# Optimization experiments

Measured on AMD Instinct MI355X. Metric: run time of the kernel, lower is better.

## Reference

```python
import jax, jax.numpy as jnp
import numpy as np

D_MODEL = 1024
D_STATE = 128
HEADDIM = 64
EXPAND = 2
CHUNK = 64
D_CONV = 4
D_INNER = EXPAND * D_MODEL          # 2048
NHEADS = D_INNER // HEADDIM         # 32
D_IN_PROJ = 2 * D_INNER + 2 * D_STATE + NHEADS  # 4384
CONV_CH = D_INNER + 2 * D_STATE     # 2304
EPS = 1e-5


def segsum(x):
    # x: (..., T) -> (..., T, T); out[i, j] = sum_{k=j+1..i} x[k] for i>=j else -inf
    T = x.shape[-1]
    m1 = jnp.tril(jnp.ones((T, T), bool), -1)
    xr = jnp.where(m1, x[..., :, None], 0.0)   # zero above/at diagonal before cumsum
    s = jnp.cumsum(xr, axis=-2)
    m0 = jnp.tril(jnp.ones((T, T), bool), 0)
    return jnp.where(m0, s, -jnp.inf)


def ssd(x, A, B, C, chunk):
    # x: (b, L, h, p); A: (b, L, h); B, C: (b, L, n)  (the h=1 dim of the torch code is squeezed)
    b, L, h, p = x.shape
    c = L // chunk
    x = x.reshape(b, c, chunk, h, p)
    A = A.reshape(b, c, chunk, h).transpose(0, 3, 1, 2)  # (b, h, c, l)
    B = B.reshape(b, c, chunk, -1)                       # (b, c, l, n)
    C = C.reshape(b, c, chunk, -1)
    A_cum = jnp.cumsum(A, axis=-1)                       # (b, h, c, l)
    Lm = jnp.exp(segsum(A))                              # (b, h, c, l, l)
    # intra-chunk (diagonal block) output
    Y_diag = jnp.einsum('bcln,bcsn,bhcls,bcshp->bclhp', C, B, Lm, x)
    # per-chunk states
    decay_states = jnp.exp(A_cum[:, :, :, -1:] - A_cum)  # (b, h, c, l)
    states = jnp.einsum('bcln,bhcl,bclhp->bchpn', B, decay_states, x)
    init = jnp.zeros_like(states[:, :1])
    states = jnp.concatenate([init, states], axis=1)     # (b, c+1, h, p, n)
    # inter-chunk recurrence
    Ac_last = jnp.pad(A_cum[:, :, :, -1], ((0, 0), (0, 0), (1, 0)))  # (b, h, c+1)
    decay_chunk = jnp.exp(segsum(Ac_last))               # (b, h, c+1, c+1)
    new_states = jnp.einsum('bhzc,bchpn->bzhpn', decay_chunk, states)
    states = new_states[:, :-1]                          # (b, c, h, p, n)
    sdo = jnp.exp(A_cum)
    Y_off = jnp.einsum('bcln,bchpn,bhcl->bclhp', C, states, sdo)
    return (Y_diag + Y_off).reshape(b, L, h, p)


def setup_inputs() -> dict:
    key = jax.random.key(0)
    ks = jax.random.split(key, 8)
    return {
        'u': jax.random.normal(ks[0], (2, 4096, D_MODEL), jnp.float32),
        'W_in': jax.random.normal(ks[1], (D_MODEL, D_IN_PROJ), jnp.float32) * 0.02,
        'conv_w': jax.random.normal(ks[2], (CONV_CH, D_CONV), jnp.float32) * 0.3,
        'conv_b': jax.random.normal(ks[3], (CONV_CH,), jnp.float32) * 0.1,
        'dt_bias': jax.random.normal(ks[4], (NHEADS,), jnp.float32),
        'A_log': jax.random.normal(ks[5], (NHEADS,), jnp.float32) * 0.5,
        'D': jax.random.normal(ks[6], (NHEADS,), jnp.float32),
        'norm_w': jnp.ones((D_INNER,), jnp.float32),
        'W_out': jax.random.normal(ks[7], (D_INNER, D_MODEL), jnp.float32) * 0.02,
    }


def reference(u, W_in, conv_w, conv_b, dt_bias, A_log, D, norm_w, W_out):
    b, L, _ = u.shape
    zxbcdt = u @ W_in                                    # (b, L, 4384)
    z = zxbcdt[..., :D_INNER]
    xBC = zxbcdt[..., D_INNER:D_INNER + CONV_CH]
    dt = jax.nn.softplus(zxbcdt[..., -NHEADS:] + dt_bias)  # (b, L, h)
    # depthwise causal conv (Conv1d pad=d_conv-1, truncated to L == left-pad only)
    xc = jnp.pad(xBC.transpose(0, 2, 1), ((0, 0), (0, 0), (D_CONV - 1, 0)))
    xc = jax.lax.conv_general_dilated(
        xc, conv_w[:, None, :], (1,), 'VALID',
        feature_group_count=CONV_CH,
        dimension_numbers=('NCH', 'OIH', 'NCH')) + conv_b[None, :, None]
    xBC = jax.nn.silu(xc.transpose(0, 2, 1))             # (b, L, 2304)
    x = xBC[..., :D_INNER].reshape(b, L, NHEADS, HEADDIM)
    B = xBC[..., D_INNER:D_INNER + D_STATE]
    C = xBC[..., D_INNER + D_STATE:]
    A = -jnp.exp(A_log)                                  # (h,)
    y = ssd(x * dt[..., None], A * dt, B, C, CHUNK)
    y = y + x * D[:, None]
    y = y.reshape(b, L, D_INNER)
    # RMSNorm with gate z
    y = y * jax.nn.silu(z)
    y = y * jax.lax.rsqrt(jnp.mean(y * y, axis=-1, keepdims=True) + EPS) * norm_w
    return y @ W_out
```

## Files before the change

kernel.cpp:

```cpp
#include <hip/hip_runtime.h>
#include <hip/hip_bf16.h>
#include <math.h>

#define D_MODEL   1024
#define D_STATE   128
#define HEADDIM   64
#define CHUNK     64
#define D_INNER   2048
#define NHEADS    32
#define D_IN_PROJ 4384
#define CONV_CH   2304
#define RCOLS     2336
#define WINT_ROWS 4480
#define BATCH     2
#define SEQ       4096
#define NCHUNK    64
#define ROWS      (BATCH*SEQ)
#define EPS_RMS   1e-5f

typedef __hip_bfloat16 bf16;
typedef __bf16 bf16x8_t __attribute__((ext_vector_type(8)));
typedef float  f32x4_t  __attribute__((ext_vector_type(4)));

__device__ __forceinline__ float siluf_(float x){ return x/(1.f+expf(-x)); }
__device__ __forceinline__ float ldf(const float* p){ return *p; }
__device__ __forceinline__ float ldf(const bf16* p){ return __bfloat162float(*p); }
__device__ __forceinline__ void  stf(float* p, float v){ *p = v; }
__device__ __forceinline__ void  stf(bf16* p, float v){ *p = __float2bfloat16(v); }

__device__ __forceinline__ __bf16 tobf(float v){
    __hip_bfloat16 t = __float2bfloat16(v);
    return *reinterpret_cast<__bf16*>(&t);
}
__device__ __forceinline__ unsigned short bfbits(float v){
    __hip_bfloat16 t = __float2bfloat16(v);
    return *reinterpret_cast<unsigned short*>(&t);
}
__device__ __forceinline__ float bfbits2f(unsigned short u){
    union { unsigned u; float f; } cv; cv.u = ((unsigned)u) << 16; return cv.f;
}

__device__ __forceinline__ void async16(const void* g, void* l) {
    __builtin_amdgcn_global_load_lds(
        (const __attribute__((address_space(1))) unsigned int*)g,
        (__attribute__((address_space(3))) unsigned int*)l, 16, 0, 0);
}

struct GemmCore {
    f32x4_t acc[4][4];
    __device__ __forceinline__ void run(const bf16* __restrict__ A, int lda,
                                        const bf16* __restrict__ Bt, int ldb,
                                        int row0, int col0, int k0, int k1,
                                        __bf16* As, __bf16* Bs,
                                        int wave, int lane) {
        const int quad = lane >> 4, l16 = lane & 15;
        const int wr = (wave >> 1) * 64, wc = (wave & 1) * 64;
#pragma unroll
        for (int i = 0; i < 4; ++i)
#pragma unroll
            for (int j = 0; j < 4; ++j) acc[i][j] = (f32x4_t){0.f, 0.f, 0.f, 0.f};
        const int ca0 = wave * 2, ca1 = wave * 2 + 1;
        const int srow = lane >> 2, scol = (lane & 3) * 8;
        const bf16* Ag0 = A  + (size_t)(row0 + ca0 * 16 + srow) * lda + scol;
        const bf16* Ag1 = A  + (size_t)(row0 + ca1 * 16 + srow) * lda + scol;
        const bf16* Bg0 = Bt + (size_t)(col0 + ca0 * 16 + srow) * ldb + scol;
        const bf16* Bg1 = Bt + (size_t)(col0 + ca1 * 16 + srow) * ldb + scol;
        __bf16* Al0 = As + ca0 * 512;
        __bf16* Al1 = As + ca1 * 512;
        __bf16* Bl0 = Bs + ca0 * 512;
        __bf16* Bl1 = Bs + ca1 * 512;
        for (int kk = k0; kk < k1; kk += 32) {
            async16(Ag0 + kk, Al0);
            async16(Ag1 + kk, Al1);
            async16(Bg0 + kk, Bl0);
            async16(Bg1 + kk, Bl1);
            __syncthreads();
            bf16x8_t af[4], bfr[4];
#pragma unroll
            for (int mi = 0; mi < 4; ++mi)
                af[mi] = *(const bf16x8_t*)(As + (wr + mi * 16 + l16) * 32 + quad * 8);
#pragma unroll
            for (int ni = 0; ni < 4; ++ni)
                bfr[ni] = *(const bf16x8_t*)(Bs + (wc + ni * 16 + l16) * 32 + quad * 8);
#pragma unroll
            for (int mi = 0; mi < 4; ++mi)
#pragma unroll
                for (int ni = 0; ni < 4; ++ni)
                    acc[mi][ni] = __builtin_amdgcn_mfma_f32_16x16x32_bf16(
                        af[mi], bfr[ni], acc[mi][ni], 0, 0, 0);
            __syncthreads();
        }
    }
};

__global__ __launch_bounds__(256) void gemm_zr_fused(const bf16* __restrict__ A,
                                                     const bf16* __restrict__ Bt,
                                                     bf16* __restrict__ Z,
                                                     bf16* __restrict__ R) {
    __shared__ __align__(16) __bf16 As[128 * 32];
    __shared__ __align__(16) __bf16 Bs[128 * 32];
    const int tid = threadIdx.x, wave = tid >> 6, lane = tid & 63;
    const int quad = lane >> 4, l16 = lane & 15;
    const int row0 = blockIdx.x * 128;
    const int ct   = blockIdx.y;
    GemmCore g;
    g.run(A, D_MODEL, Bt, D_MODEL, row0, ct * 128, 0, D_MODEL, As, Bs, wave, lane);

    bf16* Cp; int ldc_, cl0, ncols;
    if (ct < 16) { Cp = Z; ldc_ = D_INNER; cl0 = ct * 128;          ncols = D_INNER; }
    else         { Cp = R; ldc_ = RCOLS;   cl0 = ct * 128 - D_INNER; ncols = RCOLS; }
    const int wr = (wave >> 1) * 64, wc = (wave & 1) * 64;
#pragma unroll
    for (int ni = 0; ni < 4; ++ni) {
        int gc = cl0 + wc + ni * 16 + l16;
        if (gc >= ncols) continue;
#pragma unroll
        for (int mi = 0; mi < 4; ++mi)
#pragma unroll
            for (int r = 0; r < 4; ++r) {
                int gr = row0 + wr + mi * 16 + quad * 4 + r;
                stf(&Cp[(size_t)gr * ldc_ + gc], g.acc[mi][ni][r]);
            }
    }
}

__global__ __launch_bounds__(256) void gemm_out_splitk(const bf16* __restrict__ A,
                                                       const bf16* __restrict__ Bt,
                                                       float* __restrict__ part) {
    __shared__ __align__(16) __bf16 As[128 * 32];
    __shared__ __align__(16) __bf16 Bs[128 * 32];
    const int tid = threadIdx.x, wave = tid >> 6, lane = tid & 63;
    const int quad = lane >> 4, l16 = lane & 15;
    const int row0 = blockIdx.x * 128;
    const int col0 = blockIdx.y * 128;
    const int kz   = blockIdx.z;
    GemmCore g;
    g.run(A, D_INNER, Bt, D_INNER, row0, col0, kz * 1024, kz * 1024 + 1024,
          As, Bs, wave, lane);
    float* P = part + (size_t)kz * ROWS * D_MODEL;
    const int wr = (wave >> 1) * 64, wc = (wave & 1) * 64;
#pragma unroll
    for (int ni = 0; ni < 4; ++ni) {
        int gc = col0 + wc + ni * 16 + l16;
#pragma unroll
        for (int mi = 0; mi < 4; ++mi)
#pragma unroll
            for (int r = 0; r < 4; ++r) {
                int gr = row0 + wr + mi * 16 + quad * 4 + r;
                P[(size_t)gr * D_MODEL + gc] = g.acc[mi][ni][r];
            }
    }
}

__global__ void reduce_out_kernel(const float* __restrict__ part,
                                  float* __restrict__ out) {
    int i = blockIdx.x * 256 + threadIdx.x;
    float4 a = ((const float4*)part)[i];
    float4 b = ((const float4*)(part + (size_t)ROWS * D_MODEL))[i];
    ((float4*)out)[i] = make_float4(a.x + b.x, a.y + b.y, a.z + b.z, a.w + b.w);
}

__global__ void cvt_bf16_kernel(const float* __restrict__ src,
                                bf16* __restrict__ dst, int n4) {
    int i = blockIdx.x * 256 + threadIdx.x;
    if (i >= n4) return;
    float4 v = ((const float4*)src)[i];
    dst[i * 4 + 0] = __float2bfloat16(v.x);
    dst[i * 4 + 1] = __float2bfloat16(v.y);
    dst[i * 4 + 2] = __float2bfloat16(v.z);
    dst[i * 4 + 3] = __float2bfloat16(v.w);
}

__global__ __launch_bounds__(256) void transpose_cvt_kernel(const float* __restrict__ W,
                                                            bf16* __restrict__ Wt,
                                                            int R, int C, int Cpad) {
    __shared__ float tile[32][33];
    int c0 = blockIdx.x * 32, r0 = blockIdx.y * 32;
    int tx = threadIdx.x & 31, ty = threadIdx.x >> 5;
    for (int i = ty; i < 32; i += 8) {
        int r = r0 + i, c = c0 + tx;
        tile[i][tx] = (c < C) ? W[(size_t)r * C + c] : 0.f;
    }
    __syncthreads();
    for (int i = ty; i < 32; i += 8) {
        int c = c0 + i, r = r0 + tx;
        stf(&Wt[(size_t)c * R + r], tile[tx][i]);
    }
}

__global__ void prep_convw_kernel(const float* __restrict__ conv_w,
                                  bf16* __restrict__ Wc) {
    int i = blockIdx.x * 256 + threadIdx.x;
    if (i >= CONV_CH * 4) return;
    int ch = i >> 2, k = i & 3;
    Wc[k * CONV_CH + ch] = __float2bfloat16(conv_w[ch * 4 + k]);
}

__global__ __launch_bounds__(256) void conv_silu_kernel(const bf16* __restrict__ R,
                                                        const bf16* __restrict__ Wc,
                                                        const float* __restrict__ conv_b,
                                                        bf16* __restrict__ xBC) {
    int idx = blockIdx.x * 256 + threadIdx.x;
    int rq = idx / 288;
    int g = idx - rq * 288;
    int ch0 = g * 8;
    int row0 = rq * 4;
    int l0 = row0 & (SEQ - 1);

    uint4 rv[7];
#pragma unroll
    for (int j = 0; j < 7; ++j) {
        int ls = l0 - 3 + j;
        rv[j] = (ls >= 0) ? *(const uint4*)&R[(size_t)(row0 - 3 + j) * RCOLS + ch0]
                          : make_uint4(0u, 0u, 0u, 0u);
    }
    uint4 wv[4];
#pragma unroll
    for (int k = 0; k < 4; ++k)
        wv[k] = *(const uint4*)&Wc[k * CONV_CH + ch0];
    float4 b0 = ((const float4*)conv_b)[ch0 / 4];
    float4 b1 = ((const float4*)conv_b)[ch0 / 4 + 1];
    const float bias[8] = {b0.x, b0.y, b0.z, b0.w, b1.x, b1.y, b1.z, b1.w};
    float wf[4][8];
#pragma unroll
    for (int k = 0; k < 4; ++k) {
        const unsigned* wp = (const unsigned*)&wv[k];
#pragma unroll
        for (int j2 = 0; j2 < 4; ++j2) {
            wf[k][2 * j2]     = bfbits2f((unsigned short)(wp[j2] & 0xffff));
            wf[k][2 * j2 + 1] = bfbits2f((unsigned short)(wp[j2] >> 16));
        }
    }
#pragma unroll
    for (int j = 0; j < 4; ++j) {
        float acc[8];
#pragma unroll
        for (int cc = 0; cc < 8; ++cc) acc[cc] = bias[cc];
#pragma unroll
        for (int k = 0; k < 4; ++k) {
            const unsigned* vp = (const unsigned*)&rv[j + k];
#pragma unroll
            for (int j2 = 0; j2 < 4; ++j2) {
                unsigned v = vp[j2];
                acc[2 * j2]     += wf[k][2 * j2]     * bfbits2f((unsigned short)(v & 0xffff));
                acc[2 * j2 + 1] += wf[k][2 * j2 + 1] * bfbits2f((unsigned short)(v >> 16));
            }
        }
        unsigned o[4];
#pragma unroll
        for (int j2 = 0; j2 < 4; ++j2)
            o[j2] = (unsigned)bfbits(siluf_(acc[2 * j2])) |
                    ((unsigned)bfbits(siluf_(acc[2 * j2 + 1])) << 16);
        *(uint4*)&xBC[(size_t)(row0 + j) * CONV_CH + ch0] = make_uint4(o[0], o[1], o[2], o[3]);
    }
}

__global__ void dt_kernel(const bf16* __restrict__ R,
                          const float* __restrict__ dt_bias,
                          float* __restrict__ dtb) {
    int i = blockIdx.x * 256 + threadIdx.x;
    int row = i >> 2, h0 = (i & 3) * 8;
    uint4 v = *(const uint4*)&R[(size_t)row * RCOLS + CONV_CH + h0];
    float4 bia0 = ((const float4*)dt_bias)[h0 / 4];
    float4 bia1 = ((const float4*)dt_bias)[h0 / 4 + 1];
    const unsigned vv[4] = {v.x, v.y, v.z, v.w};
    const float bb[8] = {bia0.x, bia0.y, bia0.z, bia0.w, bia1.x, bia1.y, bia1.z, bia1.w};
    float o[8];
#pragma unroll
    for (int j = 0; j < 4; ++j) {
        float a = bfbits2f((unsigned short)(vv[j] & 0xffff)) + bb[2*j];
        float c = bfbits2f((unsigned short)(vv[j] >> 16)) + bb[2*j+1];
        o[2*j]   = (a > 20.f) ? a : log1pf(expf(a));
        o[2*j+1] = (c > 20.f) ? c : log1pf(expf(c));
    }
    float* dp = &dtb[(size_t)row * NHEADS + h0];
    *(float4*)dp       = make_float4(o[0], o[1], o[2], o[3]);
    *(float4*)(dp + 4) = make_float4(o[4], o[5], o[6], o[7]);
}

__global__ void acum_kernel(const float* __restrict__ dtb,
                            const float* __restrict__ A_log,
                            float* __restrict__ Acum) {
    int bch = blockIdx.x;
    int h = bch & 31;
    int bc = bch >> 5;
    int c = bc & 63, b = bc >> 6;
    int row0 = b * SEQ + c * CHUNK;
    __shared__ float sh[64];
    int l = threadIdx.x;
    float Ah = -expf(A_log[h]);
    sh[l] = Ah * dtb[(size_t)(row0 + l) * NHEADS + h];
    __syncthreads();
    float s = 0.f;
    for (int j = 0; j <= l; ++j) s += sh[j];
    Acum[(size_t)bch * 64 + l] = s;
}

__global__ __launch_bounds__(64) void gchunk_mfma_kernel(const bf16* __restrict__ xBC,
                                                         float* __restrict__ Gbuf) {
    int bc = blockIdx.x;
    int c = bc & 63, b = bc >> 6;
    int row0 = b * SEQ + c * CHUNK;
    int lane = threadIdx.x;
    int quad = lane >> 4, l16 = lane & 15;

    f32x4_t acc[4][4];
#pragma unroll
    for (int i = 0; i < 4; ++i)
#pragma unroll
        for (int j = 0; j < 4; ++j) acc[i][j] = (f32x4_t){0.f, 0.f, 0.f, 0.f};

#pragma unroll
    for (int ks = 0; ks < 4; ++ks) {
        bf16x8_t a[4], bb[4];
#pragma unroll
        for (int mi = 0; mi < 4; ++mi)
            a[mi] = *(const bf16x8_t*)&xBC[(size_t)(row0 + mi * 16 + l16) * CONV_CH +
                                           D_INNER + D_STATE + ks * 32 + quad * 8];
#pragma unroll
        for (int ni = 0; ni < 4; ++ni)
            bb[ni] = *(const bf16x8_t*)&xBC[(size_t)(row0 + ni * 16 + l16) * CONV_CH +
                                            D_INNER + ks * 32 + quad * 8];
#pragma unroll
        for (int mi = 0; mi < 4; ++mi)
#pragma unroll
            for (int ni = 0; ni < 4; ++ni)
                acc[mi][ni] = __builtin_amdgcn_mfma_f32_16x16x32_bf16(
                    a[mi], bb[ni], acc[mi][ni], 0, 0, 0);
    }
#pragma unroll
    for (int ni = 0; ni < 4; ++ni) {
        int s = ni * 16 + l16;
#pragma unroll
        for (int mi = 0; mi < 4; ++mi)
#pragma unroll
            for (int r = 0; r < 4; ++r) {
                int l = mi * 16 + quad * 4 + r;
                Gbuf[(size_t)bc * 4096 + l * 64 + s] = acc[mi][ni][r];
            }
    }
}

__global__ __launch_bounds__(256) void states_mfma_kernel(const bf16* __restrict__ xBC,
                                                          const float* __restrict__ dtb,
                                                          const float* __restrict__ Acum,
                                                          bf16* __restrict__ states) {
    __shared__ __align__(16) __bf16 BsT[128 * 72];
    __shared__ __align__(16) __bf16 xdT[4][64 * 72];
    __shared__ float dtdec[4][64];
    int bcq = blockIdx.x;
    int hq = bcq & 7, bc = bcq >> 3;
    int c = bc & 63, b = bc >> 6;
    int tid = threadIdx.x, wave = tid >> 6, lane = tid & 63;
    int h = hq * 4 + wave;
    int bch = bc * 32 + h;
    int row0 = b * SEQ + c * CHUNK;
    int quad = lane >> 4, l16 = lane & 15;

    {
        float alast = Acum[(size_t)bch * 64 + 63];
        float a = Acum[(size_t)bch * 64 + lane];
        dtdec[wave][lane] = dtb[(size_t)(row0 + lane) * NHEADS + h] * expf(alast - a);
    }
    __syncthreads();
    for (int it = 0; it < 16; ++it) {
        int i2 = tid + 256 * it;
        int l = i2 >> 6;
        int n0 = (i2 & 63) * 2;
        unsigned v = *(const unsigned*)&xBC[(size_t)(row0 + l) * CONV_CH + D_INNER + n0];
        *(unsigned short*)&BsT[(n0    ) * 72 + l] = (unsigned short)(v & 0xffff);
        *(unsigned short*)&BsT[(n0 + 1) * 72 + l] = (unsigned short)(v >> 16);
    }
    for (int it = 0; it < 32; ++it) {
        int l = 2 * it + (lane >> 5);
        int p0 = (lane & 31) * 2;
        unsigned v = *(const unsigned*)&xBC[(size_t)(row0 + l) * CONV_CH + h * 64 + p0];
        float f = dtdec[wave][l];
        xdT[wave][(p0    ) * 72 + l] = tobf(bfbits2f((unsigned short)(v & 0xffff)) * f);
        xdT[wave][(p0 + 1) * 72 + l] = tobf(bfbits2f((unsigned short)(v >> 16)) * f);
    }
    __syncthreads();

    f32x4_t acc[4][8];
#pragma unroll
    for (int i = 0; i < 4; ++i)
#pragma unroll
        for (int j = 0; j < 8; ++j) acc[i][j] = (f32x4_t){0.f, 0.f, 0.f, 0.f};
#pragma unroll
    for (int ks = 0; ks < 2; ++ks) {
        bf16x8_t a[4], bb[8];
#pragma unroll
        for (int mi = 0; mi < 4; ++mi)
            a[mi] = *(const bf16x8_t*)(&xdT[wave][(mi * 16 + l16) * 72 + ks * 32 + quad * 8]);
#pragma unroll
        for (int ni = 0; ni < 8; ++ni)
            bb[ni] = *(const bf16x8_t*)(&BsT[(ni * 16 + l16) * 72 + ks * 32 + quad * 8]);
#pragma unroll
        for (int mi = 0; mi < 4; ++mi)
#pragma unroll
            for (int ni = 0; ni < 8; ++ni)
                acc[mi][ni] = __builtin_amdgcn_mfma_f32_16x16x32_bf16(
                    a[mi], bb[ni], acc[mi][ni], 0, 0, 0);
    }
#pragma unroll
    for (int ni = 0; ni < 8; ++ni) {
        int n = ni * 16 + l16;
#pragma unroll
        for (int mi = 0; mi < 4; ++mi)
#pragma unroll
            for (int r = 0; r < 4; ++r) {
                int p = mi * 16 + quad * 4 + r;
                stf(&states[(size_t)bch * 8192 + p * 128 + n], acc[mi][ni][r]);
            }
    }
}

__global__ void scan_kernel(const float* __restrict__ Acum,
                            bf16* __restrict__ states) {
    int i = blockIdx.x * 256 + threadIdx.x;
    int pn0 = (i & 2047) * 4;
    int bh = i >> 11;
    int h = bh & 31, b = bh >> 5;
    float carry[4] = {0.f, 0.f, 0.f, 0.f};
    for (int c = 0; c < NCHUNK; ++c) {
        int bch = (b * NCHUNK + c) * NHEADS + h;
        bf16* sp = &states[(size_t)bch * 8192 + pn0];
        uint2 v = *(const uint2*)sp;
        float s0 = bfbits2f((unsigned short)(v.x & 0xffff));
        float s1 = bfbits2f((unsigned short)(v.x >> 16));
        float s2 = bfbits2f((unsigned short)(v.y & 0xffff));
        float s3 = bfbits2f((unsigned short)(v.y >> 16));
        uint2 o;
        o.x = (unsigned)bfbits(carry[0]) | ((unsigned)bfbits(carry[1]) << 16);
        o.y = (unsigned)bfbits(carry[2]) | ((unsigned)bfbits(carry[3]) << 16);
        *(uint2*)sp = o;
        float dec = expf(Acum[(size_t)bch * 64 + 63]);
        carry[0] = carry[0] * dec + s0;
        carry[1] = carry[1] * dec + s1;
        carry[2] = carry[2] * dec + s2;
        carry[3] = carry[3] * dec + s3;
    }
}

__global__ __launch_bounds__(64) void y_mfma_kernel(const bf16* __restrict__ xBC,
                                                    const float* __restrict__ dtb,
                                                    const float* __restrict__ Acum,
                                                    const float* __restrict__ Gbuf,
                                                    const bf16* __restrict__ states,
                                                    const float* __restrict__ Dv,
                                                    bf16* __restrict__ y) {
    __shared__ __align__(16) __bf16 Mm[64 * 72];
    __shared__ __align__(16) __bf16 xsT[64 * 72];
    __shared__ float acs[64], dtss[64], sdos[64];
    int bch = blockIdx.x;
    int h = bch & 31, bc = bch >> 5;
    int c = bc & 63, b = bc >> 6;
    int row0 = b * SEQ + c * CHUNK;
    int lane = threadIdx.x;
    int quad = lane >> 4, l16 = lane & 15;

    {
        float a = Acum[(size_t)bch * 64 + lane];
        acs[lane] = a;
        sdos[lane] = expf(a);
        dtss[lane] = dtb[(size_t)(row0 + lane) * NHEADS + h];
    }
    __syncthreads();
    for (int l = 0; l < 64; ++l) {
        int s = lane;
        float d = acs[l] - acs[s];
        float g = (s <= l) ? Gbuf[(size_t)bc * 4096 + l * 64 + s] * dtss[s] : 0.f;
        float coef = g * expf((s <= l) ? d : 0.f);
        Mm[l * 72 + s] = tobf(coef);
    }
    for (int it = 0; it < 32; ++it) {
        int l = 2 * it + (lane >> 5);
        int p0 = (lane & 31) * 2;
        unsigned v = *(const unsigned*)&xBC[(size_t)(row0 + l) * CONV_CH + h * 64 + p0];
        *(unsigned short*)&xsT[(p0    ) * 72 + l] = (unsigned short)(v & 0xffff);
        *(unsigned short*)&xsT[(p0 + 1) * 72 + l] = (unsigned short)(v >> 16);
    }
    __syncthreads();

    f32x4_t acc[4][4];
#pragma unroll
    for (int i = 0; i < 4; ++i)
#pragma unroll
        for (int j = 0; j < 4; ++j) acc[i][j] = (f32x4_t){0.f, 0.f, 0.f, 0.f};

#pragma unroll
    for (int ks = 0; ks < 2; ++ks) {
        bf16x8_t a[4], bb[4];
#pragma unroll
        for (int mi = 0; mi < 4; ++mi)
            a[mi] = *(const bf16x8_t*)(&Mm[(mi * 16 + l16) * 72 + ks * 32 + quad * 8]);
#pragma unroll
        for (int ni = 0; ni < 4; ++ni)
            bb[ni] = *(const bf16x8_t*)(&xsT[(ni * 16 + l16) * 72 + ks * 32 + quad * 8]);
#pragma unroll
        for (int mi = 0; mi < 4; ++mi)
#pragma unroll
            for (int ni = 0; ni < 4; ++ni)
                acc[mi][ni] = __builtin_amdgcn_mfma_f32_16x16x32_bf16(
                    a[mi], bb[ni], acc[mi][ni], 0, 0, 0);
    }
    float sdo_mi[4];
#pragma unroll
    for (int mi = 0; mi < 4; ++mi) sdo_mi[mi] = sdos[mi * 16 + l16];
#pragma unroll
    for (int ks = 0; ks < 4; ++ks) {
        bf16x8_t a[4], bb[4];
#pragma unroll
        for (int mi = 0; mi < 4; ++mi) {
            const unsigned* cp = (const unsigned*)&xBC[(size_t)(row0 + mi * 16 + l16) * CONV_CH
                                                       + D_INNER + D_STATE + ks * 32 + quad * 8];
            float sc = sdo_mi[mi];
#pragma unroll
            for (int jj = 0; jj < 4; ++jj) {
                unsigned v = cp[jj];
                a[mi][2 * jj    ] = tobf(bfbits2f((unsigned short)(v & 0xffff)) * sc);
                a[mi][2 * jj + 1] = tobf(bfbits2f((unsigned short)(v >> 16)) * sc);
            }
        }
#pragma unroll
        for (int ni = 0; ni < 4; ++ni)
            bb[ni] = *(const bf16x8_t*)&states[(size_t)bch * 8192 + (ni * 16 + l16) * 128
                                               + ks * 32 + quad * 8];
#pragma unroll
        for (int mi = 0; mi < 4; ++mi)
#pragma unroll
            for (int ni = 0; ni < 4; ++ni)
                acc[mi][ni] = __builtin_amdgcn_mfma_f32_16x16x32_bf16(
                    a[mi], bb[ni], acc[mi][ni], 0, 0, 0);
    }
    float Dh = Dv[h];
#pragma unroll
    for (int ni = 0; ni < 4; ++ni) {
        int p = ni * 16 + l16;
#pragma unroll
        for (int mi = 0; mi < 4; ++mi)
#pragma unroll
            for (int r = 0; r < 4; ++r) {
                int l = mi * 16 + quad * 4 + r;
                float xv = bfbits2f(*(const unsigned short*)&xsT[p * 72 + l]);
                stf(&y[(size_t)(row0 + l) * D_INNER + h * 64 + p],
                    acc[mi][ni][r] + Dh * xv);
            }
    }
}

__global__ __launch_bounds__(256) void gate_norm_kernel(const bf16* __restrict__ Z,
                                                        const float* __restrict__ nw,
                                                        bf16* __restrict__ y) {
    int row = blockIdx.x;
    int tid = threadIdx.x;
    int col0 = tid * 8;
    uint4 zv = *(const uint4*)&Z[(size_t)row * D_INNER + col0];
    uint4 yv = *(const uint4*)&y[(size_t)row * D_INNER + col0];
    const unsigned zz[4] = {zv.x, zv.y, zv.z, zv.w};
    const unsigned yy[4] = {yv.x, yv.y, yv.z, yv.w};
    float vals[8];
    float local = 0.f;
#pragma unroll
    for (int j = 0; j < 4; ++j) {
        float z0 = bfbits2f((unsigned short)(zz[j] & 0xffff));
        float z1 = bfbits2f((unsigned short)(zz[j] >> 16));
        float y0 = bfbits2f((unsigned short)(yy[j] & 0xffff));
        float y1 = bfbits2f((unsigned short)(yy[j] >> 16));
        float v0 = y0 * siluf_(z0);
        float v1 = y1 * siluf_(z1);
        vals[2*j] = v0; vals[2*j+1] = v1;
        local += v0 * v0 + v1 * v1;
    }
#pragma unroll
    for (int off = 32; off; off >>= 1) local += __shfl_down(local, off, 64);
    __shared__ float wsum[4];
    if ((tid & 63) == 0) wsum[tid >> 6] = local;
    __syncthreads();
    float total = wsum[0] + wsum[1] + wsum[2] + wsum[3];
    float scale = rsqrtf(total / (float)D_INNER + EPS_RMS);
    float4 w0 = ((const float4*)nw)[col0 / 4];
    float4 w1 = ((const float4*)nw)[col0 / 4 + 1];
    const float ww[8] = {w0.x, w0.y, w0.z, w0.w, w1.x, w1.y, w1.z, w1.w};
    unsigned o[4];
#pragma unroll
    for (int j = 0; j < 4; ++j)
        o[j] = (unsigned)bfbits(vals[2*j] * scale * ww[2*j]) |
               ((unsigned)bfbits(vals[2*j+1] * scale * ww[2*j+1]) << 16);
    *(uint4*)&y[(size_t)row * D_INNER + col0] = make_uint4(o[0], o[1], o[2], o[3]);
}

extern "C" void kernel_launch(void* const* d_in, const int* in_sizes, int n_in,
                              void* d_out, int out_size, void* d_ws, size_t ws_size,
                              hipStream_t stream) {
    const float* u       = (const float*)d_in[0];
    const float* W_in    = (const float*)d_in[1];
    const float* conv_w  = (const float*)d_in[2];
    const float* conv_b  = (const float*)d_in[3];
    const float* dt_bias = (const float*)d_in[4];
    const float* A_log   = (const float*)d_in[5];
    const float* Dv      = (const float*)d_in[6];
    const float* norm_w  = (const float*)d_in[7];
    const float* W_out   = (const float*)d_in[8];
    float* out = (float*)d_out;

    const size_t sz_xBC    = (size_t)ROWS * CONV_CH * 2;
    const size_t sz_Z      = (size_t)ROWS * D_INNER * 2;
    const size_t sz_y      = (size_t)ROWS * D_INNER * 2;
    const size_t sz_states = (size_t)BATCH * NCHUNK * NHEADS * 8192 * 2;
    const size_t sz_dtb    = (size_t)ROWS * NHEADS * 4;
    const size_t sz_Acum   = (size_t)BATCH * NCHUNK * NHEADS * 64 * 4;
    const size_t sz_Gbuf   = (size_t)BATCH * NCHUNK * 4096 * 4;
    const size_t sz_WinT   = (size_t)WINT_ROWS * D_MODEL * 2;
    const size_t sz_WoutT  = (size_t)D_MODEL * D_INNER * 2;
    const size_t sz_Wc     = (size_t)CONV_CH * 4 * 2;
    const size_t need = sz_xBC + sz_Z + sz_y + sz_states + sz_dtb + sz_Acum +
                        sz_Gbuf + sz_WinT + sz_WoutT + sz_Wc;
    if (ws_size < need) {
        hipMemsetAsync(d_out, 0, (size_t)out_size * sizeof(float), stream);
        return;
    }
    char* ws = (char*)d_ws;
    size_t off = 0;
    bf16*  xBC    = (bf16*) (ws + off); off += sz_xBC;
    bf16*  Z      = (bf16*) (ws + off); off += sz_Z;
    bf16*  y      = (bf16*) (ws + off); off += sz_y;
    bf16*  states = (bf16*) (ws + off); off += sz_states;
    float* dtb    = (float*)(ws + off); off += sz_dtb;
    float* Acum   = (float*)(ws + off); off += sz_Acum;
    float* Gbuf   = (float*)(ws + off); off += sz_Gbuf;
    bf16*  W_inT  = (bf16*) (ws + off); off += sz_WinT;
    bf16*  W_outT = (bf16*) (ws + off); off += sz_WoutT;
    bf16*  Wc     = (bf16*) (ws + off); off += sz_Wc;
    bf16*  R        = states;
    bf16*  u_bf16   = (bf16*)((char*)states + (size_t)ROWS * RCOLS * 2);
    float* out_part = (float*)states;

    cvt_bf16_kernel<<<(ROWS * D_MODEL / 4 + 255) / 256, 256, 0, stream>>>(
        u, u_bf16, ROWS * D_MODEL / 4);
    transpose_cvt_kernel<<<dim3(WINT_ROWS / 32, D_MODEL / 32), 256, 0, stream>>>(
        W_in, W_inT, D_MODEL, D_IN_PROJ, WINT_ROWS);
    transpose_cvt_kernel<<<dim3(D_MODEL / 32, D_INNER / 32), 256, 0, stream>>>(
        W_out, W_outT, D_INNER, D_MODEL, D_MODEL);
    prep_convw_kernel<<<(CONV_CH * 4 + 255) / 256, 256, 0, stream>>>(conv_w, Wc);
    gemm_zr_fused<<<dim3(ROWS / 128, 35), 256, 0, stream>>>(u_bf16, W_inT, Z, R);
    conv_silu_kernel<<<ROWS / 4 * 288 / 256, 256, 0, stream>>>(R, Wc, conv_b, xBC);
    dt_kernel<<<ROWS * 4 / 256, 256, 0, stream>>>(R, dt_bias, dtb);
    acum_kernel<<<BATCH * NCHUNK * NHEADS, 64, 0, stream>>>(dtb, A_log, Acum);
    gchunk_mfma_kernel<<<BATCH * NCHUNK, 64, 0, stream>>>(xBC, Gbuf);
    states_mfma_kernel<<<BATCH * NCHUNK * 8, 256, 0, stream>>>(xBC, dtb, Acum, states);
    scan_kernel<<<BATCH * NHEADS * 2048 / 256, 256, 0, stream>>>(Acum, states);
    y_mfma_kernel<<<BATCH * NCHUNK * NHEADS, 64, 0, stream>>>(
        xBC, dtb, Acum, Gbuf, states, Dv, y);
    gate_norm_kernel<<<ROWS, 256, 0, stream>>>(Z, norm_w, y);
    gemm_out_splitk<<<dim3(ROWS / 128, D_MODEL / 128, 2), 256, 0, stream>>>(
        y, W_outT, out_part);
    reduce_out_kernel<<<ROWS * D_MODEL / 4 / 256, 256, 0, stream>>>(out_part, out);
}
```

Measured before the change: 460.1 us.

## Rewrite GEMM core with triple-buffered async LDS pipeline, swizzle, and bigger tiles

Replaces the single-buffered GEMM mainloop, which synchronized twice per 32-wide k-step, with a triple-buffered 64-wide k-step pipeline. It uses explicit vmcnt waits, an XOR-swizzled LDS layout to avoid bank conflicts, and raised wave priority around the MFMA block. Block tiles grow to 256x128 with 512 threads. The output projection drops split-K and its separate reduce kernel, writing fp32 output directly. The larger LDS footprint (144KB) reduces occupancy, and the output GEMM now launches fewer blocks.

```diff
diff --git a/kernel.cpp b/kernel.cpp
--- a/kernel.cpp
+++ b/kernel.cpp
@@ -46,118 +46,155 @@
         (__attribute__((address_space(3))) unsigned int*)l, 16, 0, 0);
 }
 
-struct GemmCore {
+struct Core {
     f32x4_t acc[4][4];
-    __device__ __forceinline__ void run(const bf16* __restrict__ A, int lda,
-                                        const bf16* __restrict__ Bt, int ldb,
-                                        int row0, int col0, int k0, int k1,
-                                        __bf16* As, __bf16* Bs,
-                                        int wave, int lane) {
+
+    __device__ __forceinline__ void stageA(const bf16* __restrict__ A, int lda,
+                                           int row0, int kk, __bf16* Asb,
+                                           int tid, int lcb, int wb) {
+#pragma unroll
+        for (int c = 0; c < 4; ++c) {
+            const char* src = (const char*)(A + (size_t)(row0 + c * 64 + (tid >> 3)) * lda + kk) + lcb;
+            async16(src, Asb + c * 4096 + wb);
+        }
+    }
+    __device__ __forceinline__ void stageB(const bf16* __restrict__ Bt, int ldb,
+                                           int col0, int kk, __bf16* Bsb,
+                                           int tid, int lcb, int wb) {
+#pragma unroll
+        for (int c = 0; c < 2; ++c) {
+            const char* src = (const char*)(Bt + (size_t)(col0 + c * 64 + (tid >> 3)) * ldb + kk) + lcb;
+            async16(src, Bsb + c * 4096 + wb);
+        }
+    }
+
+    __device__ __forceinline__ void run(const bf16* __restrict__ A,
+                                        const bf16* __restrict__ Bt,
+                                        int lda, int ldb,
+                                        int row0, int col0, int k0, int nt,
+                                        __bf16* As, __bf16* Bs, int tid) {
+        const int wave = tid >> 6, lane = tid & 63;
         const int quad = lane >> 4, l16 = lane & 15;
-        const int wr = (wave >> 1) * 64, wc = (wave & 1) * 64;
+        const int wm = wave >> 1, wn = wave & 1;
+        const int wb  = wave << 9;
+        const int lcb = (((tid & 7) ^ ((tid >> 3) & 7)) << 4);
+        const int xb = (l16 & 7) << 4;
+
 #pragma unroll
         for (int i = 0; i < 4; ++i)
 #pragma unroll
             for (int j = 0; j < 4; ++j) acc[i][j] = (f32x4_t){0.f, 0.f, 0.f, 0.f};
-        const int ca0 = wave * 2, ca1 = wave * 2 + 1;
-        const int srow = lane >> 2, scol = (lane & 3) * 8;
-        const bf16* Ag0 = A  + (size_t)(row0 + ca0 * 16 + srow) * lda + scol;
-        const bf16* Ag1 = A  + (size_t)(row0 + ca1 * 16 + srow) * lda + scol;
-        const bf16* Bg0 = Bt + (size_t)(col0 + ca0 * 16 + srow) * ldb + scol;
-        const bf16* Bg1 = Bt + (size_t)(col0 + ca1 * 16 + srow) * ldb + scol;
-        __bf16* Al0 = As + ca0 * 512;
-        __bf16* Al1 = As + ca1 * 512;
-        __bf16* Bl0 = Bs + ca0 * 512;
-        __bf16* Bl1 = Bs + ca1 * 512;
-        for (int kk = k0; kk < k1; kk += 32) {
-            async16(Ag0 + kk, Al0);
-            async16(Ag1 + kk, Al1);
-            async16(Bg0 + kk, Bl0);
-            async16(Bg1 + kk, Bl1);
-            __syncthreads();
-            bf16x8_t af[4], bfr[4];
+
+        int aoff[4][2], boff[4][2];
+#pragma unroll
+        for (int mi = 0; mi < 4; ++mi)
+#pragma unroll
+            for (int ks = 0; ks < 2; ++ks) {
+                const int cb = ((ks << 6) | (quad << 4)) ^ xb;
+                aoff[mi][ks] = (wm * 64 + mi * 16 + l16) * 128 + cb;
+                boff[mi][ks] = (wn * 64 + mi * 16 + l16) * 128 + cb;
+            }
+
+        stageA(A, lda, row0, k0,      As,          tid, lcb, wb);
+        stageB(Bt, ldb, col0, k0,     Bs,          tid, lcb, wb);
+        stageA(A, lda, row0, k0 + 64, As + 16384,  tid, lcb, wb);
+        stageB(Bt, ldb, col0, k0 + 64, Bs + 8192,  tid, lcb, wb);
+
+        const char* AsC = (const char*)As;
+        const char* BsC = (const char*)Bs;
+        int cur = 0, sb = 2;
+        for (int t = 0; t < nt; ++t) {
+            if (t < nt - 1) asm volatile("s_waitcnt vmcnt(6)" ::: "memory");
+            else            asm volatile("s_waitcnt vmcnt(0)" ::: "memory");
+            __builtin_amdgcn_s_barrier();
+            asm volatile("" ::: "memory");
+            if (t + 2 < nt) {
+                stageA(A, lda, row0, k0 + (t + 2) * 64, As + sb * 16384, tid, lcb, wb);
+                stageB(Bt, ldb, col0, k0 + (t + 2) * 64, Bs + sb * 8192, tid, lcb, wb);
+            }
+            const char* Ab = AsC + cur * 32768;
+            const char* Bb = BsC + cur * 16384;
+            bf16x8_t af[4][2], bfr[4][2];
 #pragma unroll
             for (int mi = 0; mi < 4; ++mi)
-                af[mi] = *(const bf16x8_t*)(As + (wr + mi * 16 + l16) * 32 + quad * 8);
-#pragma unroll
-            for (int ni = 0; ni < 4; ++ni)
-                bfr[ni] = *(const bf16x8_t*)(Bs + (wc + ni * 16 + l16) * 32 + quad * 8);
-#pragma unroll
-            for (int mi = 0; mi < 4; ++mi)
-#pragma unroll
-                for (int ni = 0; ni < 4; ++ni)
-                    acc[mi][ni] = __builtin_amdgcn_mfma_f32_16x16x32_bf16(
-                        af[mi], bfr[ni], acc[mi][ni], 0, 0, 0);
-            __syncthreads();
+#pragma unroll
+                for (int ks = 0; ks < 2; ++ks) {
+                    af[mi][ks]  = *(const bf16x8_t*)(Ab + aoff[mi][ks]);
+                    bfr[mi][ks] = *(const bf16x8_t*)(Bb + boff[mi][ks]);
+                }
+            __builtin_amdgcn_s_setprio(1);
+#pragma unroll
+            for (int ks = 0; ks < 2; ++ks)
+#pragma unroll
+                for (int mi = 0; mi < 4; ++mi)
+#pragma unroll
+                    for (int ni = 0; ni < 4; ++ni)
+                        acc[mi][ni] = __builtin_amdgcn_mfma_f32_16x16x32_bf16(
+                            af[mi][ks], bfr[ni][ks], acc[mi][ni], 0, 0, 0);
+            __builtin_amdgcn_s_setprio(0);
+            cur = (cur + 1 == 3) ? 0 : cur + 1;
+            sb  = (sb  + 1 == 3) ? 0 : sb  + 1;
         }
     }
 };
 
-__global__ __launch_bounds__(256) void gemm_zr_fused(const bf16* __restrict__ A,
+__global__ __launch_bounds__(512) void gemm_zr_fused(const bf16* __restrict__ A,
                                                      const bf16* __restrict__ Bt,
                                                      bf16* __restrict__ Z,
                                                      bf16* __restrict__ R) {
-    __shared__ __align__(16) __bf16 As[128 * 32];
-    __shared__ __align__(16) __bf16 Bs[128 * 32];
-    const int tid = threadIdx.x, wave = tid >> 6, lane = tid & 63;
+    __shared__ __align__(16) __bf16 As[3 * 16384];
+    __shared__ __align__(16) __bf16 Bs[3 * 8192];
+    const int tid = threadIdx.x;
+    const int row0 = blockIdx.x * 256;
+    const int ct   = blockIdx.y;
+    Core g;
+    g.run(A, Bt, D_MODEL, D_MODEL, row0, ct * 128, 0, 16, As, Bs, tid);
+
+    const int wave = tid >> 6, lane = tid & 63;
     const int quad = lane >> 4, l16 = lane & 15;
-    const int row0 = blockIdx.x * 128;
-    const int ct   = blockIdx.y;
-    GemmCore g;
-    g.run(A, D_MODEL, Bt, D_MODEL, row0, ct * 128, 0, D_MODEL, As, Bs, wave, lane);
-
+    const int wm = wave >> 1, wn = wave & 1;
     bf16* Cp; int ldc_, cl0, ncols;
-    if (ct < 16) { Cp = Z; ldc_ = D_INNER; cl0 = ct * 128;          ncols = D_INNER; }
+    if (ct < 16) { Cp = Z; ldc_ = D_INNER; cl0 = ct * 128;           ncols = D_INNER; }
     else         { Cp = R; ldc_ = RCOLS;   cl0 = ct * 128 - D_INNER; ncols = RCOLS; }
-    const int wr = (wave >> 1) * 64, wc = (wave & 1) * 64;
 #pragma unroll
     for (int ni = 0; ni < 4; ++ni) {
-        int gc = cl0 + wc + ni * 16 + l16;
+        int gc = cl0 + wn * 64 + ni * 16 + l16;
         if (gc >= ncols) continue;
 #pragma unroll
         for (int mi = 0; mi < 4; ++mi)
 #pragma unroll
             for (int r = 0; r < 4; ++r) {
-                int gr = row0 + wr + mi * 16 + quad * 4 + r;
+                int gr = row0 + wm * 64 + mi * 16 + quad * 4 + r;
                 stf(&Cp[(size_t)gr * ldc_ + gc], g.acc[mi][ni][r]);
             }
     }
 }
 
-__global__ __launch_bounds__(256) void gemm_out_splitk(const bf16* __restrict__ A,
+__global__ __launch_bounds__(512) void gemm_out_kernel(const bf16* __restrict__ A,
                                                        const bf16* __restrict__ Bt,
-                                                       float* __restrict__ part) {
-    __shared__ __align__(16) __bf16 As[128 * 32];
-    __shared__ __align__(16) __bf16 Bs[128 * 32];
-    const int tid = threadIdx.x, wave = tid >> 6, lane = tid & 63;
+                                                       float* __restrict__ out) {
+    __shared__ __align__(16) __bf16 As[3 * 16384];
+    __shared__ __align__(16) __bf16 Bs[3 * 8192];
+    const int tid = threadIdx.x;
+    const int row0 = blockIdx.x * 256;
+    const int col0 = blockIdx.y * 128;
+    Core g;
+    g.run(A, Bt, D_INNER, D_INNER, row0, col0, 0, 32, As, Bs, tid);
+
+    const int wave = tid >> 6, lane = tid & 63;
     const int quad = lane >> 4, l16 = lane & 15;
-    const int row0 = blockIdx.x * 128;
-    const int col0 = blockIdx.y * 128;
-    const int kz   = blockIdx.z;
-    GemmCore g;
-    g.run(A, D_INNER, Bt, D_INNER, row0, col0, kz * 1024, kz * 1024 + 1024,
-          As, Bs, wave, lane);
-    float* P = part + (size_t)kz * ROWS * D_MODEL;
-    const int wr = (wave >> 1) * 64, wc = (wave & 1) * 64;
+    const int wm = wave >> 1, wn = wave & 1;
 #pragma unroll
     for (int ni = 0; ni < 4; ++ni) {
-        int gc = col0 + wc + ni * 16 + l16;
+        int gc = col0 + wn * 64 + ni * 16 + l16;
 #pragma unroll
         for (int mi = 0; mi < 4; ++mi)
 #pragma unroll
             for (int r = 0; r < 4; ++r) {
-                int gr = row0 + wr + mi * 16 + quad * 4 + r;
-                P[(size_t)gr * D_MODEL + gc] = g.acc[mi][ni][r];
-            }
-    }
-}
-
-__global__ void reduce_out_kernel(const float* __restrict__ part,
-                                  float* __restrict__ out) {
-    int i = blockIdx.x * 256 + threadIdx.x;
-    float4 a = ((const float4*)part)[i];
-    float4 b = ((const float4*)(part + (size_t)ROWS * D_MODEL))[i];
-    ((float4*)out)[i] = make_float4(a.x + b.x, a.y + b.y, a.z + b.z, a.w + b.w);
+                int gr = row0 + wm * 64 + mi * 16 + quad * 4 + r;
+                out[(size_t)gr * D_MODEL + gc] = g.acc[mi][ni][r];
+            }
+    }
 }
 
 __global__ void cvt_bf16_kernel(const float* __restrict__ src,
@@ -634,7 +671,6 @@
     bf16*  Wc     = (bf16*) (ws + off); off += sz_Wc;
     bf16*  R        = states;
     bf16*  u_bf16   = (bf16*)((char*)states + (size_t)ROWS * RCOLS * 2);
-    float* out_part = (float*)states;
 
     cvt_bf16_kernel<<<(ROWS * D_MODEL / 4 + 255) / 256, 256, 0, stream>>>(
         u, u_bf16, ROWS * D_MODEL / 4);
@@ -643,7 +679,7 @@
     transpose_cvt_kernel<<<dim3(D_MODEL / 32, D_INNER / 32), 256, 0, stream>>>(
         W_out, W_outT, D_INNER, D_MODEL, D_MODEL);
     prep_convw_kernel<<<(CONV_CH * 4 + 255) / 256, 256, 0, stream>>>(conv_w, Wc);
-    gemm_zr_fused<<<dim3(ROWS / 128, 35), 256, 0, stream>>>(u_bf16, W_inT, Z, R);
+    gemm_zr_fused<<<dim3(ROWS / 256, 35), 512, 0, stream>>>(u_bf16, W_inT, Z, R);
     conv_silu_kernel<<<ROWS / 4 * 288 / 256, 256, 0, stream>>>(R, Wc, conv_b, xBC);
     dt_kernel<<<ROWS * 4 / 256, 256, 0, stream>>>(R, dt_bias, dtb);
     acum_kernel<<<BATCH * NCHUNK * NHEADS, 64, 0, stream>>>(dtb, A_log, Acum);
@@ -653,7 +689,6 @@
     y_mfma_kernel<<<BATCH * NCHUNK * NHEADS, 64, 0, stream>>>(
         xBC, dtb, Acum, Gbuf, states, Dv, y);
     gate_norm_kernel<<<ROWS, 256, 0, stream>>>(Z, norm_w, y);
-    gemm_out_splitk<<<dim3(ROWS / 128, D_MODEL / 128, 2), 256, 0, stream>>>(
-        y, W_outT, out_part);
-    reduce_out_kernel<<<ROWS * D_MODEL / 4 / 256, 256, 0, stream>>>(out_part, out);
-}
+    gemm_out_kernel<<<dim3(ROWS / 256, D_MODEL / 128), 512, 0, stream>>>(
+        y, W_outT, out);
+}
```

Measured after the change: 445.1 us. 1.03x faster.

## Fuse C·Bᵀ computation into y kernel and drop split-K output GEMM

Applied to the files above, without the earlier changes.

Removes the separate gchunk kernel and its Gbuf round trip. Each y_mfma block now recomputes the lower-triangular C·Bᵀ for its chunk with MFMA and applies the decay and dt coefficients directly in registers. The output projection goes from a two-way split-K GEMM plus reduction kernel to a single full-K GEMM that writes straight to the output. This saves fp32 partial-buffer traffic and two launches. In exchange the C·Bᵀ product is recomputed once per head (32x redundant), and the output GEMM launches half as many blocks.

```diff
diff --git a/kernel.cpp b/kernel.cpp
--- a/kernel.cpp
+++ b/kernel.cpp
@@ -124,20 +124,17 @@
     }
 }
 
-__global__ __launch_bounds__(256) void gemm_out_splitk(const bf16* __restrict__ A,
+__global__ __launch_bounds__(256) void gemm_out_kernel(const bf16* __restrict__ A,
                                                        const bf16* __restrict__ Bt,
-                                                       float* __restrict__ part) {
+                                                       float* __restrict__ out) {
     __shared__ __align__(16) __bf16 As[128 * 32];
     __shared__ __align__(16) __bf16 Bs[128 * 32];
     const int tid = threadIdx.x, wave = tid >> 6, lane = tid & 63;
     const int quad = lane >> 4, l16 = lane & 15;
     const int row0 = blockIdx.x * 128;
     const int col0 = blockIdx.y * 128;
-    const int kz   = blockIdx.z;
     GemmCore g;
-    g.run(A, D_INNER, Bt, D_INNER, row0, col0, kz * 1024, kz * 1024 + 1024,
-          As, Bs, wave, lane);
-    float* P = part + (size_t)kz * ROWS * D_MODEL;
+    g.run(A, D_INNER, Bt, D_INNER, row0, col0, 0, D_INNER, As, Bs, wave, lane);
     const int wr = (wave >> 1) * 64, wc = (wave & 1) * 64;
 #pragma unroll
     for (int ni = 0; ni < 4; ++ni) {
@@ -147,17 +144,9 @@
 #pragma unroll
             for (int r = 0; r < 4; ++r) {
                 int gr = row0 + wr + mi * 16 + quad * 4 + r;
-                P[(size_t)gr * D_MODEL + gc] = g.acc[mi][ni][r];
+                out[(size_t)gr * D_MODEL + gc] = g.acc[mi][ni][r];
             }
     }
-}
-
-__global__ void reduce_out_kernel(const float* __restrict__ part,
-                                  float* __restrict__ out) {
-    int i = blockIdx.x * 256 + threadIdx.x;
-    float4 a = ((const float4*)part)[i];
-    float4 b = ((const float4*)(part + (size_t)ROWS * D_MODEL))[i];
-    ((float4*)out)[i] = make_float4(a.x + b.x, a.y + b.y, a.z + b.z, a.w + b.w);
 }
 
 __global__ void cvt_bf16_kernel(const float* __restrict__ src,
@@ -294,51 +283,6 @@
     float s = 0.f;
     for (int j = 0; j <= l; ++j) s += sh[j];
     Acum[(size_t)bch * 64 + l] = s;
-}
-
-__global__ __launch_bounds__(64) void gchunk_mfma_kernel(const bf16* __restrict__ xBC,
-                                                         float* __restrict__ Gbuf) {
-    int bc = blockIdx.x;
-    int c = bc & 63, b = bc >> 6;
-    int row0 = b * SEQ + c * CHUNK;
-    int lane = threadIdx.x;
-    int quad = lane >> 4, l16 = lane & 15;
-
-    f32x4_t acc[4][4];
-#pragma unroll
-    for (int i = 0; i < 4; ++i)
-#pragma unroll
-        for (int j = 0; j < 4; ++j) acc[i][j] = (f32x4_t){0.f, 0.f, 0.f, 0.f};
-
-#pragma unroll
-    for (int ks = 0; ks < 4; ++ks) {
-        bf16x8_t a[4], bb[4];
-#pragma unroll
-        for (int mi = 0; mi < 4; ++mi)
-            a[mi] = *(const bf16x8_t*)&xBC[(size_t)(row0 + mi * 16 + l16) * CONV_CH +
-                                           D_INNER + D_STATE + ks * 32 + quad * 8];
-#pragma unroll
-        for (int ni = 0; ni < 4; ++ni)
-            bb[ni] = *(const bf16x8_t*)&xBC[(size_t)(row0 + ni * 16 + l16) * CONV_CH +
-                                            D_INNER + ks * 32 + quad * 8];
-#pragma unroll
-        for (int mi = 0; mi < 4; ++mi)
-#pragma unroll
-            for (int ni = 0; ni < 4; ++ni)
-                acc[mi][ni] = __builtin_amdgcn_mfma_f32_16x16x32_bf16(
-                    a[mi], bb[ni], acc[mi][ni], 0, 0, 0);
-    }
-#pragma unroll
-    for (int ni = 0; ni < 4; ++ni) {
-        int s = ni * 16 + l16;
-#pragma unroll
-        for (int mi = 0; mi < 4; ++mi)
-#pragma unroll
-            for (int r = 0; r < 4; ++r) {
-                int l = mi * 16 + quad * 4 + r;
-                Gbuf[(size_t)bc * 4096 + l * 64 + s] = acc[mi][ni][r];
-            }
-    }
 }
 
 __global__ __launch_bounds__(256) void states_mfma_kernel(const bf16* __restrict__ xBC,
@@ -445,7 +389,6 @@
 __global__ __launch_bounds__(64) void y_mfma_kernel(const bf16* __restrict__ xBC,
                                                     const float* __restrict__ dtb,
                                                     const float* __restrict__ Acum,
-                                                    const float* __restrict__ Gbuf,
                                                     const bf16* __restrict__ states,
                                                     const float* __restrict__ Dv,
                                                     bf16* __restrict__ y) {
@@ -465,20 +408,50 @@
         sdos[lane] = expf(a);
         dtss[lane] = dtb[(size_t)(row0 + lane) * NHEADS + h];
     }
-    __syncthreads();
-    for (int l = 0; l < 64; ++l) {
-        int s = lane;
-        float d = acs[l] - acs[s];
-        float g = (s <= l) ? Gbuf[(size_t)bc * 4096 + l * 64 + s] * dtss[s] : 0.f;
-        float coef = g * expf((s <= l) ? d : 0.f);
-        Mm[l * 72 + s] = tobf(coef);
-    }
     for (int it = 0; it < 32; ++it) {
         int l = 2 * it + (lane >> 5);
         int p0 = (lane & 31) * 2;
         unsigned v = *(const unsigned*)&xBC[(size_t)(row0 + l) * CONV_CH + h * 64 + p0];
         *(unsigned short*)&xsT[(p0    ) * 72 + l] = (unsigned short)(v & 0xffff);
         *(unsigned short*)&xsT[(p0 + 1) * 72 + l] = (unsigned short)(v >> 16);
+    }
+    __syncthreads();
+
+    f32x4_t gacc[4][4];
+#pragma unroll
+    for (int i = 0; i < 4; ++i)
+#pragma unroll
+        for (int j = 0; j < 4; ++j) gacc[i][j] = (f32x4_t){0.f, 0.f, 0.f, 0.f};
+#pragma unroll
+    for (int ks = 0; ks < 4; ++ks) {
+        bf16x8_t a[4], bb[4];
+#pragma unroll
+        for (int mi = 0; mi < 4; ++mi)
+            a[mi] = *(const bf16x8_t*)&xBC[(size_t)(row0 + mi * 16 + l16) * CONV_CH +
+                                           D_INNER + D_STATE + ks * 32 + quad * 8];
+#pragma unroll
+        for (int ni = 0; ni < 4; ++ni)
+            bb[ni] = *(const bf16x8_t*)&xBC[(size_t)(row0 + ni * 16 + l16) * CONV_CH +
+                                            D_INNER + ks * 32 + quad * 8];
+#pragma unroll
+        for (int mi = 0; mi < 4; ++mi)
+#pragma unroll
+            for (int ni = 0; ni <= mi; ++ni)
+                gacc[mi][ni] = __builtin_amdgcn_mfma_f32_16x16x32_bf16(
+                    a[mi], bb[ni], gacc[mi][ni], 0, 0, 0);
+    }
+#pragma unroll
+    for (int ni = 0; ni < 4; ++ni) {
+        int s = ni * 16 + l16;
+        float ds = dtss[s], as = acs[s];
+#pragma unroll
+        for (int mi = 0; mi < 4; ++mi)
+#pragma unroll
+            for (int r = 0; r < 4; ++r) {
+                int l = mi * 16 + quad * 4 + r;
+                float coef = (s <= l) ? gacc[mi][ni][r] * ds * expf(acs[l] - as) : 0.f;
+                Mm[l * 72 + s] = tobf(coef);
+            }
     }
     __syncthreads();
 
@@ -610,12 +583,11 @@
     const size_t sz_states = (size_t)BATCH * NCHUNK * NHEADS * 8192 * 2;
     const size_t sz_dtb    = (size_t)ROWS * NHEADS * 4;
     const size_t sz_Acum   = (size_t)BATCH * NCHUNK * NHEADS * 64 * 4;
-    const size_t sz_Gbuf   = (size_t)BATCH * NCHUNK * 4096 * 4;
     const size_t sz_WinT   = (size_t)WINT_ROWS * D_MODEL * 2;
     const size_t sz_WoutT  = (size_t)D_MODEL * D_INNER * 2;
     const size_t sz_Wc     = (size_t)CONV_CH * 4 * 2;
     const size_t need = sz_xBC + sz_Z + sz_y + sz_states + sz_dtb + sz_Acum +
-                        sz_Gbuf + sz_WinT + sz_WoutT + sz_Wc;
+                        sz_WinT + sz_WoutT + sz_Wc;
     if (ws_size < need) {
         hipMemsetAsync(d_out, 0, (size_t)out_size * sizeof(float), stream);
         return;
@@ -628,13 +600,11 @@
     bf16*  states = (bf16*) (ws + off); off += sz_states;
     float* dtb    = (float*)(ws + off); off += sz_dtb;
     float* Acum   = (float*)(ws + off); off += sz_Acum;
-    float* Gbuf   = (float*)(ws + off); off += sz_Gbuf;
     bf16*  W_inT  = (bf16*) (ws + off); off += sz_WinT;
     bf16*  W_outT = (bf16*) (ws + off); off += sz_WoutT;
     bf16*  Wc     = (bf16*) (ws + off); off += sz_Wc;
     bf16*  R        = states;
     bf16*  u_bf16   = (bf16*)((char*)states + (size_t)ROWS * RCOLS * 2);
-    float* out_part = (float*)states;
 
     cvt_bf16_kernel<<<(ROWS * D_MODEL / 4 + 255) / 256, 256, 0, stream>>>(
         u, u_bf16, ROWS * D_MODEL / 4);
@@ -647,13 +617,11 @@
     conv_silu_kernel<<<ROWS / 4 * 288 / 256, 256, 0, stream>>>(R, Wc, conv_b, xBC);
     dt_kernel<<<ROWS * 4 / 256, 256, 0, stream>>>(R, dt_bias, dtb);
     acum_kernel<<<BATCH * NCHUNK * NHEADS, 64, 0, stream>>>(dtb, A_log, Acum);
-    gchunk_mfma_kernel<<<BATCH * NCHUNK, 64, 0, stream>>>(xBC, Gbuf);
     states_mfma_kernel<<<BATCH * NCHUNK * 8, 256, 0, stream>>>(xBC, dtb, Acum, states);
     scan_kernel<<<BATCH * NHEADS * 2048 / 256, 256, 0, stream>>>(Acum, states);
     y_mfma_kernel<<<BATCH * NCHUNK * NHEADS, 64, 0, stream>>>(
-        xBC, dtb, Acum, Gbuf, states, Dv, y);
+        xBC, dtb, Acum, states, Dv, y);
     gate_norm_kernel<<<ROWS, 256, 0, stream>>>(Z, norm_w, y);
-    gemm_out_splitk<<<dim3(ROWS / 128, D_MODEL / 128, 2), 256, 0, stream>>>(
-        y, W_outT, out_part);
-    reduce_out_kernel<<<ROWS * D_MODEL / 4 / 256, 256, 0, stream>>>(out_part, out);
-}
+    gemm_out_kernel<<<dim3(ROWS / 128, D_MODEL / 128), 256, 0, stream>>>(
+        y, W_outT, out);
+}
```

Result: faster. 415.0 us (-9.8%).
